# Kernel optimization log

Measured on AMD Instinct MI355X. Metric: run time of the kernel, lower is better.

The kernel has to match this reference:

```python
import jax, jax.numpy as jnp
import numpy as np

N, T, F_IN = 20000, 8, 64
FILTERS, HEADS = 32, 4
E = 320000
LEAKY = 0.2  # PyG GATConv default negative_slope
HID = HEADS * FILTERS  # 128


def setup_inputs() -> dict:
    key = jax.random.key(0)
    ks = jax.random.split(key, 16)
    g = lambda k, shape, scale: jax.random.normal(k, shape, dtype=jnp.float32) * scale
    return {
        "x": g(ks[0], (N, T, F_IN), 1.0),
        "edge_index": jax.random.randint(ks[1], (2, E), 0, N, dtype=jnp.int32),
        # GATConv 1: lin weight, attention vectors (per head), bias
        "W1": g(ks[2], (HID, F_IN), (2.0 / F_IN) ** 0.5),
        "att_src1": g(ks[3], (HEADS, FILTERS), 0.1),
        "att_dst1": g(ks[4], (HEADS, FILTERS), 0.1),
        "b1": jnp.zeros((HID,), jnp.float32),
        # GATConv 2
        "W2": g(ks[5], (HID, HID), (2.0 / HID) ** 0.5),
        "att_src2": g(ks[6], (HEADS, FILTERS), 0.1),
        "att_dst2": g(ks[7], (HEADS, FILTERS), 0.1),
        "b2": jnp.zeros((HID,), jnp.float32),
        # MLP head
        "lw1": g(ks[8], (FILTERS, HID), (2.0 / HID) ** 0.5),
        "lb1": jnp.zeros((FILTERS,), jnp.float32),
        "lw2": g(ks[9], (1, FILTERS), (2.0 / FILTERS) ** 0.5),
        "lb2": jnp.zeros((1,), jnp.float32),
    }


def gat_layer(x, src, dst, W, a_src, a_dst, b):
    """PyG GATConv (concat=True, add_self_loops already applied to src/dst)."""
    h = (x @ W.T).reshape(N, HEADS, FILTERS)          # [N,H,F]
    es = (h * a_src).sum(-1)                          # [N,H] per-node src score
    ed = (h * a_dst).sum(-1)                          # [N,H] per-node dst score
    e = jax.nn.leaky_relu(es[src] + ed[dst], LEAKY)   # [E',H]
    # segment softmax over incoming edges per destination node
    m = jax.ops.segment_max(e, dst, num_segments=N)
    ex = jnp.exp(e - m[dst])
    denom = jax.ops.segment_sum(ex, dst, num_segments=N)
    alpha = ex / (denom[dst] + 1e-16)                 # [E',H]
    out = jax.ops.segment_sum(h[src] * alpha[:, :, None], dst, num_segments=N)
    return out.reshape(N, HID) + b


def reference(x, edge_index, W1, att_src1, att_dst1, b1,
              W2, att_src2, att_dst2, b2, lw1, lb1, lw2, lb2):
    # add self loops (PyG GATConv default add_self_loops=True)
    loop = jnp.arange(N, dtype=edge_index.dtype)
    src = jnp.concatenate([edge_index[0], loop])
    dst = jnp.concatenate([edge_index[1], loop])

    def step(_, x_t):
        h = jax.nn.elu(gat_layer(x_t, src, dst, W1, att_src1, att_dst1, b1))
        # dropout is identity in eval mode
        h = jax.nn.elu(gat_layer(h, src, dst, W2, att_src2, att_dst2, b2))
        h = jax.nn.relu(h @ lw1.T + lb1)
        y = h @ lw2.T + lb2                            # [N,1]
        return None, y

    _, ys = jax.lax.scan(step, None, jnp.transpose(x, (1, 0, 2)))  # scan over T
    return ys  # [T, N, 1] (stacked version of the original list of outputs)
```

## Files before the change

kernel.cpp:

```cpp
#include <hip/hip_runtime.h>

constexpr int cN     = 20000;
constexpr int cT     = 8;
constexpr int cFIN   = 64;
constexpr int cHEADS = 4;
constexpr int cF     = 32;
constexpr int cHID   = 128;
constexpr int cE     = 320000;
constexpr int cET    = cE + cN;
constexpr int cR     = cN * cT;
constexpr float cLEAKY = 0.2f;

typedef __attribute__((ext_vector_type(8))) short bf16x8;
typedef __attribute__((ext_vector_type(4))) float f32x4;

static __device__ __forceinline__ unsigned short f2bfu(float f) {
    unsigned int u;
    __builtin_memcpy(&u, &f, 4);
    u += 0x7FFFu + ((u >> 16) & 1u);
    return (unsigned short)(u >> 16);
}
static __device__ __forceinline__ void unpack2(unsigned int v, float& lo, float& hi) {
    unsigned int ul = v << 16, uh = v & 0xFFFF0000u;
    __builtin_memcpy(&lo, &ul, 4);
    __builtin_memcpy(&hi, &uh, 4);
}
static __device__ __forceinline__ unsigned int pack2(float lo, float hi) {
    unsigned int ul, uh;
    __builtin_memcpy(&ul, &lo, 4);
    __builtin_memcpy(&uh, &hi, 4);
    ul += 0x7FFFu + ((ul >> 16) & 1u);
    uh += 0x7FFFu + ((uh >> 16) & 1u);
    return (ul >> 16) | (uh & 0xFFFF0000u);
}

__global__ void cvt_w_kernel(const float* W1, const float* W2, const float* lw1,
                             unsigned short* W1b, unsigned short* W2b, unsigned short* lw1b) {
    int i = blockIdx.x * 256 + threadIdx.x;
    if (i < cHID * cFIN)                      W1b[i] = f2bfu(W1[i]);
    else if (i < cHID * cFIN + cHID * cHID)   W2b[i - cHID * cFIN] = f2bfu(W2[i - cHID * cFIN]);
    else if (i < cHID * cFIN + cHID * cHID + cF * cHID)
        lw1b[i - cHID * cFIN - cHID * cHID] = f2bfu(lw1[i - cHID * cFIN - cHID * cHID]);
}

__global__ void deg_init_kernel(int* deg) {
    int n = blockIdx.x * blockDim.x + threadIdx.x;
    if (n < cN) deg[n] = 1;
}
__global__ void deg_count_kernel(const int* ei, int* deg) {
    int e = blockIdx.x * blockDim.x + threadIdx.x;
    if (e < cE) atomicAdd(&deg[ei[cE + e]], 1);
}
__global__ void scan_kernel(const int* deg, int* offs, int* cur) {
    __shared__ int lds[256];
    const int CH = 80;
    int tid  = threadIdx.x;
    int base = tid * CH;
    int tot = 0;
    for (int j = 0; j < CH; j++) {
        int idx = base + j;
        if (idx < cN) tot += deg[idx];
    }
    lds[tid] = tot;
    __syncthreads();
    for (int off = 1; off < 256; off <<= 1) {
        int v = (tid >= off) ? lds[tid - off] : 0;
        __syncthreads();
        lds[tid] += v;
        __syncthreads();
    }
    int run = lds[tid] - tot;
    for (int j = 0; j < CH; j++) {
        int idx = base + j;
        if (idx < cN) { offs[idx] = run; cur[idx] = run; run += deg[idx]; }
    }
    if (tid == 255) offs[cN] = lds[255];
}
__global__ void scatter_kernel(const int* ei, int* cur, int* csr) {
    int e = blockIdx.x * blockDim.x + threadIdx.x;
    if (e >= cET) return;
    int s, d;
    if (e < cE) { s = ei[e]; d = ei[cE + e]; }
    else        { s = e - cE; d = s; }
    int pos = atomicAdd(&cur[d], 1);
    csr[pos] = s;
}

__global__ __launch_bounds__(256) void gemm1_fused_kernel(
        const float* __restrict__ x, const unsigned short* __restrict__ W,
        const float* __restrict__ a_src, const float* __restrict__ a_dst,
        unsigned short* __restrict__ hb, float* __restrict__ es, float* __restrict__ ed) {
    __shared__ float hl[64][132];
    int tid  = threadIdx.x;
    int wave = tid >> 6;
    int lane = tid & 63;
    int q    = lane >> 4;
    int mi   = lane & 15;
    int m0   = blockIdx.x * 64 + wave * 16;

    int rho = m0 + mi;
    int t = rho / cN;
    int n = rho - t * cN;
    const float* xr = x + (size_t)n * (cT * cFIN) + t * cFIN;

    bf16x8 afrag[2];
    #pragma unroll
    for (int s = 0; s < 2; s++) {
        float4 v0 = *(const float4*)(xr + s * 32 + q * 8);
        float4 v1 = *(const float4*)(xr + s * 32 + q * 8 + 4);
        bf16x8 f;
        f[0] = (short)f2bfu(v0.x); f[1] = (short)f2bfu(v0.y);
        f[2] = (short)f2bfu(v0.z); f[3] = (short)f2bfu(v0.w);
        f[4] = (short)f2bfu(v1.x); f[5] = (short)f2bfu(v1.y);
        f[6] = (short)f2bfu(v1.z); f[7] = (short)f2bfu(v1.w);
        afrag[s] = f;
    }

    f32x4 acc[8];
    #pragma unroll
    for (int ct = 0; ct < 8; ct++) acc[ct] = (f32x4){0.f, 0.f, 0.f, 0.f};
    #pragma unroll
    for (int ct = 0; ct < 8; ct++) {
        int c = ct * 16 + mi;
        #pragma unroll
        for (int s = 0; s < 2; s++) {
            bf16x8 bfrag = *(const bf16x8*)(W + (size_t)c * cFIN + s * 32 + q * 8);
            acc[ct] = __builtin_amdgcn_mfma_f32_16x16x32_bf16(afrag[s], bfrag, acc[ct], 0, 0, 0);
        }
    }

    #pragma unroll
    for (int ct = 0; ct < 8; ct++)
        #pragma unroll
        for (int r = 0; r < 4; r++)
            hl[wave * 16 + q * 4 + r][ct * 16 + mi] = acc[ct][r];
    __syncthreads();

    {
        int r2 = tid & 63;
        int hd = tid >> 6;
        int rg = blockIdx.x * 64 + r2;
        const float* hr = &hl[r2][hd * cF];
        const float* sa = a_src + hd * cF;
        const float* da = a_dst + hd * cF;
        float s1 = 0.f, s2 = 0.f;
        #pragma unroll 8
        for (int f = 0; f < cF; f++) {
            float hv = hr[f];
            s1 += hv * sa[f];
            s2 += hv * da[f];
        }
        es[rg * cHEADS + hd] = s1;
        ed[rg * cHEADS + hd] = s2;
    }

    size_t base = (size_t)blockIdx.x * 64 * cHID;
    #pragma unroll
    for (int it = 0; it < 8; it++) {
        int g   = tid + it * 256;
        int row = g >> 5;
        int c4  = (g & 31) * 4;
        float4 v = *(const float4*)&hl[row][c4];
        unsigned int p0 = pack2(v.x, v.y), p1 = pack2(v.z, v.w);
        *(uint2*)(hb + base + (size_t)row * cHID + c4) = make_uint2(p0, p1);
    }
}

__global__ __launch_bounds__(256) void gemm2_mfma_kernel(
        const unsigned short* __restrict__ A, const unsigned short* __restrict__ W,
        const float* __restrict__ a_src, const float* __restrict__ a_dst,
        unsigned short* __restrict__ hb, float* __restrict__ es, float* __restrict__ ed) {
    __shared__ float hl[64][132];
    int tid  = threadIdx.x;
    int wave = tid >> 6;
    int lane = tid & 63;
    int q    = lane >> 4;
    int mi   = lane & 15;
    int m0   = blockIdx.x * 64 + wave * 16;

    bf16x8 afrag[4];
    #pragma unroll
    for (int s = 0; s < 4; s++)
        afrag[s] = *(const bf16x8*)(A + (size_t)(m0 + mi) * cHID + s * 32 + q * 8);

    f32x4 acc[8];
    #pragma unroll
    for (int ct = 0; ct < 8; ct++) acc[ct] = (f32x4){0.f, 0.f, 0.f, 0.f};
    #pragma unroll
    for (int ct = 0; ct < 8; ct++) {
        int c = ct * 16 + mi;
        #pragma unroll
        for (int s = 0; s < 4; s++) {
            bf16x8 bfrag = *(const bf16x8*)(W + (size_t)c * cHID + s * 32 + q * 8);
            acc[ct] = __builtin_amdgcn_mfma_f32_16x16x32_bf16(afrag[s], bfrag, acc[ct], 0, 0, 0);
        }
    }

    #pragma unroll
    for (int ct = 0; ct < 8; ct++)
        #pragma unroll
        for (int r = 0; r < 4; r++)
            hl[wave * 16 + q * 4 + r][ct * 16 + mi] = acc[ct][r];
    __syncthreads();

    {
        int r2 = tid & 63;
        int hd = tid >> 6;
        int rg = blockIdx.x * 64 + r2;
        const float* hr = &hl[r2][hd * cF];
        const float* sa = a_src + hd * cF;
        const float* da = a_dst + hd * cF;
        float s1 = 0.f, s2 = 0.f;
        #pragma unroll 8
        for (int f = 0; f < cF; f++) {
            float hv = hr[f];
            s1 += hv * sa[f];
            s2 += hv * da[f];
        }
        es[rg * cHEADS + hd] = s1;
        ed[rg * cHEADS + hd] = s2;
    }

    size_t base = (size_t)blockIdx.x * 64 * cHID;
    #pragma unroll
    for (int it = 0; it < 8; it++) {
        int g   = tid + it * 256;
        int row = g >> 5;
        int c4  = (g & 31) * 4;
        float4 v = *(const float4*)&hl[row][c4];
        unsigned int p0 = pack2(v.x, v.y), p1 = pack2(v.z, v.w);
        *(uint2*)(hb + base + (size_t)row * cHID + c4) = make_uint2(p0, p1);
    }
}

__global__ __launch_bounds__(256) void agg_kernel(
        const unsigned short* __restrict__ hb, const float* __restrict__ es,
        const float* __restrict__ ed,
        const int* __restrict__ offs, const int* __restrict__ csr,
        const float* __restrict__ bias, unsigned short* __restrict__ outb) {
    int b    = blockIdx.x;
    int t    = b & 7;
    int g    = b >> 3;
    int lrow = threadIdx.x >> 4;
    int n    = g * 16 + lrow;
    int j    = threadIdx.x & 15;
    int head = j >> 2;
    int rho  = t * cN + n;
    int s0 = offs[n], s1 = offs[n + 1];
    float edn = ed[(size_t)rho * cHEADS + head];
    const char* hpc = (const char*)(hb + (size_t)t * cN * cHID);
    const char* epc = (const char*)(es + (size_t)t * cN * cHEADS);
    const char* cc  = (const char*)csr;
    unsigned jo = (unsigned)j * 16u;
    unsigned ho = (unsigned)head * 4u;

    float acc[8] = {};
    float den = 0.f;
    int i = s0;
    for (; i + 3 < s1; i += 4) {
        unsigned io = (unsigned)i * 4u;
        int sa = *(const int*)(cc + io);
        int sb = *(const int*)(cc + io + 4u);
        int sc = *(const int*)(cc + io + 8u);
        int sd = *(const int*)(cc + io + 12u);
        uint4 ra = *(const uint4*)(hpc + (((unsigned)sa) << 8) + jo);
        uint4 rb = *(const uint4*)(hpc + (((unsigned)sb) << 8) + jo);
        uint4 rc = *(const uint4*)(hpc + (((unsigned)sc) << 8) + jo);
        uint4 rd = *(const uint4*)(hpc + (((unsigned)sd) << 8) + jo);
        float ea = *(const float*)(epc + (((unsigned)sa) << 4) + ho) + edn;
        float eb = *(const float*)(epc + (((unsigned)sb) << 4) + ho) + edn;
        float ec = *(const float*)(epc + (((unsigned)sc) << 4) + ho) + edn;
        float ee = *(const float*)(epc + (((unsigned)sd) << 4) + ho) + edn;
        ea = (ea >= 0.f) ? ea : cLEAKY * ea;
        eb = (eb >= 0.f) ? eb : cLEAKY * eb;
        ec = (ec >= 0.f) ? ec : cLEAKY * ec;
        ee = (ee >= 0.f) ? ee : cLEAKY * ee;
        float wa = __expf(ea), wb = __expf(eb), wc = __expf(ec), wd = __expf(ee);
        den += wa; den += wb; den += wc; den += wd;
        float lo, hi;
        unpack2(ra.x, lo, hi); acc[0] += wa * lo; acc[1] += wa * hi;
        unpack2(ra.y, lo, hi); acc[2] += wa * lo; acc[3] += wa * hi;
        unpack2(ra.z, lo, hi); acc[4] += wa * lo; acc[5] += wa * hi;
        unpack2(ra.w, lo, hi); acc[6] += wa * lo; acc[7] += wa * hi;
        unpack2(rb.x, lo, hi); acc[0] += wb * lo; acc[1] += wb * hi;
        unpack2(rb.y, lo, hi); acc[2] += wb * lo; acc[3] += wb * hi;
        unpack2(rb.z, lo, hi); acc[4] += wb * lo; acc[5] += wb * hi;
        unpack2(rb.w, lo, hi); acc[6] += wb * lo; acc[7] += wb * hi;
        unpack2(rc.x, lo, hi); acc[0] += wc * lo; acc[1] += wc * hi;
        unpack2(rc.y, lo, hi); acc[2] += wc * lo; acc[3] += wc * hi;
        unpack2(rc.z, lo, hi); acc[4] += wc * lo; acc[5] += wc * hi;
        unpack2(rc.w, lo, hi); acc[6] += wc * lo; acc[7] += wc * hi;
        unpack2(rd.x, lo, hi); acc[0] += wd * lo; acc[1] += wd * hi;
        unpack2(rd.y, lo, hi); acc[2] += wd * lo; acc[3] += wd * hi;
        unpack2(rd.z, lo, hi); acc[4] += wd * lo; acc[5] += wd * hi;
        unpack2(rd.w, lo, hi); acc[6] += wd * lo; acc[7] += wd * hi;
    }
    for (; i < s1; i++) {
        int sa = *(const int*)(cc + (unsigned)i * 4u);
        uint4 ra = *(const uint4*)(hpc + (((unsigned)sa) << 8) + jo);
        float ea = *(const float*)(epc + (((unsigned)sa) << 4) + ho) + edn;
        ea = (ea >= 0.f) ? ea : cLEAKY * ea;
        float wa = __expf(ea);
        den += wa;
        float lo, hi;
        unpack2(ra.x, lo, hi); acc[0] += wa * lo; acc[1] += wa * hi;
        unpack2(ra.y, lo, hi); acc[2] += wa * lo; acc[3] += wa * hi;
        unpack2(ra.z, lo, hi); acc[4] += wa * lo; acc[5] += wa * hi;
        unpack2(ra.w, lo, hi); acc[6] += wa * lo; acc[7] += wa * hi;
    }
    float inv = 1.f / (den + 1e-16f);
    float4 b0 = *(const float4*)(bias + 8 * j);
    float4 b1 = *(const float4*)(bias + 8 * j + 4);
    float r0 = acc[0] * inv + b0.x; r0 = (r0 > 0.f) ? r0 : expm1f(r0);
    float r1 = acc[1] * inv + b0.y; r1 = (r1 > 0.f) ? r1 : expm1f(r1);
    float r2 = acc[2] * inv + b0.z; r2 = (r2 > 0.f) ? r2 : expm1f(r2);
    float r3 = acc[3] * inv + b0.w; r3 = (r3 > 0.f) ? r3 : expm1f(r3);
    float r4 = acc[4] * inv + b1.x; r4 = (r4 > 0.f) ? r4 : expm1f(r4);
    float r5 = acc[5] * inv + b1.y; r5 = (r5 > 0.f) ? r5 : expm1f(r5);
    float r6 = acc[6] * inv + b1.z; r6 = (r6 > 0.f) ? r6 : expm1f(r6);
    float r7 = acc[7] * inv + b1.w; r7 = (r7 > 0.f) ? r7 : expm1f(r7);
    uint4 o;
    o.x = pack2(r0, r1); o.y = pack2(r2, r3); o.z = pack2(r4, r5); o.w = pack2(r6, r7);
    *(uint4*)(outb + (size_t)rho * cHID + 8 * j) = o;
}

__global__ __launch_bounds__(256) void TemporalGAT_20005957665499_kernel(
        const unsigned short* __restrict__ X, const unsigned short* __restrict__ lw1b,
        const float* __restrict__ lb1, const float* __restrict__ lw2,
        const float* __restrict__ lb2, float* __restrict__ out) {
    int tid  = threadIdx.x;
    int wave = tid >> 6;
    int lane = tid & 63;
    int q    = lane >> 4;
    int mi   = lane & 15;
    int m0   = blockIdx.x * 64 + wave * 16;

    bf16x8 afrag[4];
    #pragma unroll
    for (int s = 0; s < 4; s++)
        afrag[s] = *(const bf16x8*)(X + (size_t)(m0 + mi) * cHID + s * 32 + q * 8);

    f32x4 acc[2];
    acc[0] = (f32x4){0.f, 0.f, 0.f, 0.f};
    acc[1] = (f32x4){0.f, 0.f, 0.f, 0.f};
    #pragma unroll
    for (int ct = 0; ct < 2; ct++) {
        int c = ct * 16 + mi;
        #pragma unroll
        for (int s = 0; s < 4; s++) {
            bf16x8 bfrag = *(const bf16x8*)(lw1b + (size_t)c * cHID + s * 32 + q * 8);
            acc[ct] = __builtin_amdgcn_mfma_f32_16x16x32_bf16(afrag[s], bfrag, acc[ct], 0, 0, 0);
        }
    }

    float lb1a = lb1[mi], lb1b_ = lb1[16 + mi];
    float lw2a = lw2[mi], lw2b_ = lw2[16 + mi];
    float l2 = lb2[0];
    #pragma unroll
    for (int r = 0; r < 4; r++) {
        float va = acc[0][r] + lb1a; va = fmaxf(va, 0.f);
        float vb = acc[1][r] + lb1b_; vb = fmaxf(vb, 0.f);
        float v = va * lw2a + vb * lw2b_;
        v += __shfl_xor(v, 1);
        v += __shfl_xor(v, 2);
        v += __shfl_xor(v, 4);
        v += __shfl_xor(v, 8);
        if (mi == 0) out[m0 + q * 4 + r] = v + l2;
    }
}

extern "C" void kernel_launch(void* const* d_in, const int* in_sizes, int n_in,
                              void* d_out, int out_size, void* d_ws, size_t ws_size,
                              hipStream_t stream) {
    const float* x   = (const float*)d_in[0];
    const int*   ei  = (const int*)d_in[1];
    const float* W1  = (const float*)d_in[2];
    const float* as1 = (const float*)d_in[3];
    const float* ad1 = (const float*)d_in[4];
    const float* b1  = (const float*)d_in[5];
    const float* W2  = (const float*)d_in[6];
    const float* as2 = (const float*)d_in[7];
    const float* ad2 = (const float*)d_in[8];
    const float* b2  = (const float*)d_in[9];
    const float* lw1 = (const float*)d_in[10];
    const float* lb1 = (const float*)d_in[11];
    const float* lw2 = (const float*)d_in[12];
    const float* lb2 = (const float*)d_in[13];
    float* out = (float*)d_out;
    (void)in_sizes; (void)n_in; (void)out_size; (void)ws_size;

    char* ws = (char*)d_ws;
    size_t o = 0;
    auto carveN = [&](size_t bytes) { void* p = ws + o; o += (bytes + 255) & ~(size_t)255; return p; };
    unsigned short* hb   = (unsigned short*)carveN((size_t)cR * cHID * 2);
    unsigned short* xb2  = (unsigned short*)carveN((size_t)cR * cHID * 2);
    unsigned short* xb3  = (unsigned short*)carveN((size_t)cR * cHID * 2);
    unsigned short* W1b  = (unsigned short*)carveN((size_t)cHID * cFIN * 2);
    unsigned short* W2b  = (unsigned short*)carveN((size_t)cHID * cHID * 2);
    unsigned short* lw1b = (unsigned short*)carveN((size_t)cF * cHID * 2);
    float* es_buf  = (float*)carveN((size_t)cR * cHEADS * 4);
    float* ed_buf  = (float*)carveN((size_t)cR * cHEADS * 4);
    int*   deg     = (int*)carveN((size_t)cN * 4);
    int*   offs    = (int*)carveN((size_t)(cN + 1) * 4);
    int*   cursor  = (int*)carveN((size_t)cN * 4);
    int*   csr     = (int*)carveN((size_t)cET * 4);

    cvt_w_kernel<<<(cHID * cFIN + cHID * cHID + cF * cHID + 255) / 256, 256, 0, stream>>>(
        W1, W2, lw1, W1b, W2b, lw1b);

    deg_init_kernel<<<(cN + 255) / 256, 256, 0, stream>>>(deg);
    deg_count_kernel<<<(cE + 255) / 256, 256, 0, stream>>>(ei, deg);
    scan_kernel<<<1, 256, 0, stream>>>(deg, offs, cursor);
    scatter_kernel<<<(cET + 255) / 256, 256, 0, stream>>>(ei, cursor, csr);

    gemm1_fused_kernel<<<cR / 64, 256, 0, stream>>>(x, W1b, as1, ad1, hb, es_buf, ed_buf);
    agg_kernel<<<(cN / 16) * cT, 256, 0, stream>>>(hb, es_buf, ed_buf, offs, csr, b1, xb2);
    gemm2_mfma_kernel<<<cR / 64, 256, 0, stream>>>(xb2, W2b, as2, ad2, hb, es_buf, ed_buf);
    agg_kernel<<<(cN / 16) * cT, 256, 0, stream>>>(hb, es_buf, ed_buf, offs, csr, b2, xb3);
    TemporalGAT_20005957665499_kernel<<<cR / 64, 256, 0, stream>>>(xb3, lw1b, lb1, lw2, lb2, out);
}
```

Before: 415.6 us.

## Fuse GAT aggregation with following GEMM and MLP head, use exp2 scaling

Fuses each attention-aggregation pass with the next dense step: the layer-1 aggregation now feeds the layer-2 GEMM and score computation through a swizzled LDS tile, and the layer-2 aggregation feeds the MLP head directly. This removes two intermediate bf16 activation round trips through global memory and two kernel launches. Attention scores are pre-scaled by log2(e) so the inner loop uses the hardware exp2 instead of __expf. The degree scan is also staged through LDS, which costs about 80KB of shared memory in a single-block kernel. The fused kernels do small 16-row MFMA tiles per block, and the head kernel leaves three of four waves idle during its GEMM.

```diff
diff --git a/kernel.cpp b/kernel.cpp
--- a/kernel.cpp
+++ b/kernel.cpp
@@ -10,6 +10,7 @@
 constexpr int cET    = cE + cN;
 constexpr int cR     = cN * cT;
 constexpr float cLEAKY = 0.2f;
+constexpr float cL2E = 1.44269504088896340736f;
 
 typedef __attribute__((ext_vector_type(8))) short bf16x8;
 typedef __attribute__((ext_vector_type(4))) float f32x4;
@@ -52,15 +53,20 @@
     if (e < cE) atomicAdd(&deg[ei[cE + e]], 1);
 }
 __global__ void scan_kernel(const int* deg, int* offs, int* cur) {
+    __shared__ int sdeg[79 * 256];
     __shared__ int lds[256];
-    const int CH = 80;
-    int tid  = threadIdx.x;
+    int tid = threadIdx.x;
+    #pragma unroll 4
+    for (int k = 0; k < 79; k++) {
+        int idx = k * 256 + tid;
+        sdeg[idx] = (idx < cN) ? deg[idx] : 0;
+    }
+    __syncthreads();
+    const int CH = 79;
     int base = tid * CH;
     int tot = 0;
-    for (int j = 0; j < CH; j++) {
-        int idx = base + j;
-        if (idx < cN) tot += deg[idx];
-    }
+    #pragma unroll 8
+    for (int j = 0; j < CH; j++) tot += sdeg[base + j];
     lds[tid] = tot;
     __syncthreads();
     for (int off = 1; off < 256; off <<= 1) {
@@ -72,7 +78,7 @@
     int run = lds[tid] - tot;
     for (int j = 0; j < CH; j++) {
         int idx = base + j;
-        if (idx < cN) { offs[idx] = run; cur[idx] = run; run += deg[idx]; }
+        if (idx < cN) { offs[idx] = run; cur[idx] = run; run += sdeg[idx]; }
     }
     if (tid == 255) offs[cN] = lds[255];
 }
@@ -150,8 +156,8 @@
             s1 += hv * sa[f];
             s2 += hv * da[f];
         }
-        es[rg * cHEADS + hd] = s1;
-        ed[rg * cHEADS + hd] = s2;
+        es[rg * cHEADS + hd] = s1 * cL2E;
+        ed[rg * cHEADS + hd] = s2 * cL2E;
     }
 
     size_t base = (size_t)blockIdx.x * 64 * cHID;
@@ -166,84 +172,11 @@
     }
 }
 
-__global__ __launch_bounds__(256) void gemm2_mfma_kernel(
-        const unsigned short* __restrict__ A, const unsigned short* __restrict__ W,
-        const float* __restrict__ a_src, const float* __restrict__ a_dst,
-        unsigned short* __restrict__ hb, float* __restrict__ es, float* __restrict__ ed) {
-    __shared__ float hl[64][132];
-    int tid  = threadIdx.x;
-    int wave = tid >> 6;
-    int lane = tid & 63;
-    int q    = lane >> 4;
-    int mi   = lane & 15;
-    int m0   = blockIdx.x * 64 + wave * 16;
-
-    bf16x8 afrag[4];
-    #pragma unroll
-    for (int s = 0; s < 4; s++)
-        afrag[s] = *(const bf16x8*)(A + (size_t)(m0 + mi) * cHID + s * 32 + q * 8);
-
-    f32x4 acc[8];
-    #pragma unroll
-    for (int ct = 0; ct < 8; ct++) acc[ct] = (f32x4){0.f, 0.f, 0.f, 0.f};
-    #pragma unroll
-    for (int ct = 0; ct < 8; ct++) {
-        int c = ct * 16 + mi;
-        #pragma unroll
-        for (int s = 0; s < 4; s++) {
-            bf16x8 bfrag = *(const bf16x8*)(W + (size_t)c * cHID + s * 32 + q * 8);
-            acc[ct] = __builtin_amdgcn_mfma_f32_16x16x32_bf16(afrag[s], bfrag, acc[ct], 0, 0, 0);
-        }
-    }
-
-    #pragma unroll
-    for (int ct = 0; ct < 8; ct++)
-        #pragma unroll
-        for (int r = 0; r < 4; r++)
-            hl[wave * 16 + q * 4 + r][ct * 16 + mi] = acc[ct][r];
-    __syncthreads();
-
-    {
-        int r2 = tid & 63;
-        int hd = tid >> 6;
-        int rg = blockIdx.x * 64 + r2;
-        const float* hr = &hl[r2][hd * cF];
-        const float* sa = a_src + hd * cF;
-        const float* da = a_dst + hd * cF;
-        float s1 = 0.f, s2 = 0.f;
-        #pragma unroll 8
-        for (int f = 0; f < cF; f++) {
-            float hv = hr[f];
-            s1 += hv * sa[f];
-            s2 += hv * da[f];
-        }
-        es[rg * cHEADS + hd] = s1;
-        ed[rg * cHEADS + hd] = s2;
-    }
-
-    size_t base = (size_t)blockIdx.x * 64 * cHID;
-    #pragma unroll
-    for (int it = 0; it < 8; it++) {
-        int g   = tid + it * 256;
-        int row = g >> 5;
-        int c4  = (g & 31) * 4;
-        float4 v = *(const float4*)&hl[row][c4];
-        unsigned int p0 = pack2(v.x, v.y), p1 = pack2(v.z, v.w);
-        *(uint2*)(hb + base + (size_t)row * cHID + c4) = make_uint2(p0, p1);
-    }
-}
-
-__global__ __launch_bounds__(256) void agg_kernel(
+static __device__ __forceinline__ void agg_core(
         const unsigned short* __restrict__ hb, const float* __restrict__ es,
-        const float* __restrict__ ed,
-        const int* __restrict__ offs, const int* __restrict__ csr,
-        const float* __restrict__ bias, unsigned short* __restrict__ outb) {
-    int b    = blockIdx.x;
-    int t    = b & 7;
-    int g    = b >> 3;
-    int lrow = threadIdx.x >> 4;
-    int n    = g * 16 + lrow;
-    int j    = threadIdx.x & 15;
+        const float* __restrict__ ed, const int* __restrict__ offs,
+        const int* __restrict__ csr, const float* __restrict__ bias,
+        int t, int n, int j, float* r) {
     int head = j >> 2;
     int rho  = t * cN + n;
     int s0 = offs[n], s1 = offs[n + 1];
@@ -275,7 +208,8 @@
         eb = (eb >= 0.f) ? eb : cLEAKY * eb;
         ec = (ec >= 0.f) ? ec : cLEAKY * ec;
         ee = (ee >= 0.f) ? ee : cLEAKY * ee;
-        float wa = __expf(ea), wb = __expf(eb), wc = __expf(ec), wd = __expf(ee);
+        float wa = __builtin_amdgcn_exp2f(ea), wb = __builtin_amdgcn_exp2f(eb);
+        float wc = __builtin_amdgcn_exp2f(ec), wd = __builtin_amdgcn_exp2f(ee);
         den += wa; den += wb; den += wc; den += wd;
         float lo, hi;
         unpack2(ra.x, lo, hi); acc[0] += wa * lo; acc[1] += wa * hi;
@@ -300,7 +234,7 @@
         uint4 ra = *(const uint4*)(hpc + (((unsigned)sa) << 8) + jo);
         float ea = *(const float*)(epc + (((unsigned)sa) << 4) + ho) + edn;
         ea = (ea >= 0.f) ? ea : cLEAKY * ea;
-        float wa = __expf(ea);
+        float wa = __builtin_amdgcn_exp2f(ea);
         den += wa;
         float lo, hi;
         unpack2(ra.x, lo, hi); acc[0] += wa * lo; acc[1] += wa * hi;
@@ -310,62 +244,167 @@
     }
     float inv = 1.f / (den + 1e-16f);
     float4 b0 = *(const float4*)(bias + 8 * j);
-    float4 b1 = *(const float4*)(bias + 8 * j + 4);
-    float r0 = acc[0] * inv + b0.x; r0 = (r0 > 0.f) ? r0 : expm1f(r0);
-    float r1 = acc[1] * inv + b0.y; r1 = (r1 > 0.f) ? r1 : expm1f(r1);
-    float r2 = acc[2] * inv + b0.z; r2 = (r2 > 0.f) ? r2 : expm1f(r2);
-    float r3 = acc[3] * inv + b0.w; r3 = (r3 > 0.f) ? r3 : expm1f(r3);
-    float r4 = acc[4] * inv + b1.x; r4 = (r4 > 0.f) ? r4 : expm1f(r4);
-    float r5 = acc[5] * inv + b1.y; r5 = (r5 > 0.f) ? r5 : expm1f(r5);
-    float r6 = acc[6] * inv + b1.z; r6 = (r6 > 0.f) ? r6 : expm1f(r6);
-    float r7 = acc[7] * inv + b1.w; r7 = (r7 > 0.f) ? r7 : expm1f(r7);
-    uint4 o;
-    o.x = pack2(r0, r1); o.y = pack2(r2, r3); o.z = pack2(r4, r5); o.w = pack2(r6, r7);
-    *(uint4*)(outb + (size_t)rho * cHID + 8 * j) = o;
-}
-
-__global__ __launch_bounds__(256) void TemporalGAT_20005957665499_kernel(
-        const unsigned short* __restrict__ X, const unsigned short* __restrict__ lw1b,
-        const float* __restrict__ lb1, const float* __restrict__ lw2,
-        const float* __restrict__ lb2, float* __restrict__ out) {
+    float4 b1v = *(const float4*)(bias + 8 * j + 4);
+    float v0 = acc[0] * inv + b0.x;  r[0] = (v0 > 0.f) ? v0 : expm1f(v0);
+    float v1 = acc[1] * inv + b0.y;  r[1] = (v1 > 0.f) ? v1 : expm1f(v1);
+    float v2 = acc[2] * inv + b0.z;  r[2] = (v2 > 0.f) ? v2 : expm1f(v2);
+    float v3 = acc[3] * inv + b0.w;  r[3] = (v3 > 0.f) ? v3 : expm1f(v3);
+    float v4 = acc[4] * inv + b1v.x; r[4] = (v4 > 0.f) ? v4 : expm1f(v4);
+    float v5 = acc[5] * inv + b1v.y; r[5] = (v5 > 0.f) ? v5 : expm1f(v5);
+    float v6 = acc[6] * inv + b1v.z; r[6] = (v6 > 0.f) ? v6 : expm1f(v6);
+    float v7 = acc[7] * inv + b1v.w; r[7] = (v7 > 0.f) ? v7 : expm1f(v7);
+}
+
+__global__ __launch_bounds__(256) void agg_gemm_kernel(
+        const unsigned short* __restrict__ hb, const float* __restrict__ es,
+        const float* __restrict__ ed, const int* __restrict__ offs,
+        const int* __restrict__ csr, const float* __restrict__ bias,
+        const unsigned short* __restrict__ W2, const float* __restrict__ a_src,
+        const float* __restrict__ a_dst, unsigned short* __restrict__ hb2,
+        float* __restrict__ es2, float* __restrict__ ed2) {
+    __shared__ unsigned short tile[16 * 128];
+    __shared__ float hl[16][132];
+    int b    = blockIdx.x;
+    int t    = b & 7;
+    int g    = b >> 3;
     int tid  = threadIdx.x;
+    int lrow = tid >> 4;
+    int j    = tid & 15;
+    int n0   = g * 16;
+
+    float r[8];
+    agg_core(hb, es, ed, offs, csr, bias, t, n0 + lrow, j, r);
+    {
+        uint4 o;
+        o.x = pack2(r[0], r[1]); o.y = pack2(r[2], r[3]);
+        o.z = pack2(r[4], r[5]); o.w = pack2(r[6], r[7]);
+        unsigned tb = (unsigned)lrow * 256u + (((unsigned)j * 16u) ^ (((unsigned)(lrow & 7)) << 4));
+        *(uint4*)((char*)tile + tb) = o;
+    }
+    __syncthreads();
+
     int wave = tid >> 6;
     int lane = tid & 63;
     int q    = lane >> 4;
     int mi   = lane & 15;
-    int m0   = blockIdx.x * 64 + wave * 16;
-
     bf16x8 afrag[4];
     #pragma unroll
-    for (int s = 0; s < 4; s++)
-        afrag[s] = *(const bf16x8*)(X + (size_t)(m0 + mi) * cHID + s * 32 + q * 8);
-
-    f32x4 acc[2];
-    acc[0] = (f32x4){0.f, 0.f, 0.f, 0.f};
-    acc[1] = (f32x4){0.f, 0.f, 0.f, 0.f};
+    for (int s = 0; s < 4; s++) {
+        unsigned addr = (unsigned)mi * 256u +
+                        (((unsigned)(s * 64 + q * 16)) ^ (((unsigned)(mi & 7)) << 4));
+        afrag[s] = *(const bf16x8*)((const char*)tile + addr);
+    }
+    f32x4 acc2[2];
+    acc2[0] = (f32x4){0.f, 0.f, 0.f, 0.f};
+    acc2[1] = (f32x4){0.f, 0.f, 0.f, 0.f};
     #pragma unroll
     for (int ct = 0; ct < 2; ct++) {
-        int c = ct * 16 + mi;
+        int c = (wave * 2 + ct) * 16 + mi;
         #pragma unroll
         for (int s = 0; s < 4; s++) {
-            bf16x8 bfrag = *(const bf16x8*)(lw1b + (size_t)c * cHID + s * 32 + q * 8);
-            acc[ct] = __builtin_amdgcn_mfma_f32_16x16x32_bf16(afrag[s], bfrag, acc[ct], 0, 0, 0);
-        }
-    }
-
-    float lb1a = lb1[mi], lb1b_ = lb1[16 + mi];
-    float lw2a = lw2[mi], lw2b_ = lw2[16 + mi];
-    float l2 = lb2[0];
-    #pragma unroll
-    for (int r = 0; r < 4; r++) {
-        float va = acc[0][r] + lb1a; va = fmaxf(va, 0.f);
-        float vb = acc[1][r] + lb1b_; vb = fmaxf(vb, 0.f);
-        float v = va * lw2a + vb * lw2b_;
-        v += __shfl_xor(v, 1);
-        v += __shfl_xor(v, 2);
-        v += __shfl_xor(v, 4);
-        v += __shfl_xor(v, 8);
-        if (mi == 0) out[m0 + q * 4 + r] = v + l2;
+            bf16x8 bfrag = *(const bf16x8*)(W2 + (size_t)c * cHID + s * 32 + q * 8);
+            acc2[ct] = __builtin_amdgcn_mfma_f32_16x16x32_bf16(afrag[s], bfrag, acc2[ct], 0, 0, 0);
+        }
+    }
+    #pragma unroll
+    for (int ct = 0; ct < 2; ct++)
+        #pragma unroll
+        for (int rr = 0; rr < 4; rr++)
+            hl[q * 4 + rr][(wave * 2 + ct) * 16 + mi] = acc2[ct][rr];
+    __syncthreads();
+
+    if (tid < 64) {
+        int r2 = tid & 15;
+        int hd = tid >> 4;
+        int rg = t * cN + n0 + r2;
+        const float* hr = &hl[r2][hd * cF];
+        const float* sa = a_src + hd * cF;
+        const float* da = a_dst + hd * cF;
+        float s1 = 0.f, s2 = 0.f;
+        #pragma unroll 8
+        for (int f = 0; f < cF; f++) {
+            float hv = hr[f];
+            s1 += hv * sa[f];
+            s2 += hv * da[f];
+        }
+        es2[(size_t)rg * cHEADS + hd] = s1 * cL2E;
+        ed2[(size_t)rg * cHEADS + hd] = s2 * cL2E;
+    }
+    {
+        int row = tid >> 4;
+        int c8  = (tid & 15) * 8;
+        float4 v0 = *(const float4*)&hl[row][c8];
+        float4 v1 = *(const float4*)&hl[row][c8 + 4];
+        uint4 o;
+        o.x = pack2(v0.x, v0.y); o.y = pack2(v0.z, v0.w);
+        o.z = pack2(v1.x, v1.y); o.w = pack2(v1.z, v1.w);
+        *(uint4*)(hb2 + (size_t)(t * cN + n0 + row) * cHID + c8) = o;
+    }
+}
+
+__global__ __launch_bounds__(256) void TemporalGAT_20005957665499_kernel(
+        const unsigned short* __restrict__ hb2, const float* __restrict__ es,
+        const float* __restrict__ ed, const int* __restrict__ offs,
+        const int* __restrict__ csr, const float* __restrict__ bias,
+        const unsigned short* __restrict__ lw1b, const float* __restrict__ lb1,
+        const float* __restrict__ lw2, const float* __restrict__ lb2,
+        float* __restrict__ out) {
+    __shared__ unsigned short tile[16 * 128];
+    int b    = blockIdx.x;
+    int t    = b & 7;
+    int g    = b >> 3;
+    int tid  = threadIdx.x;
+    int lrow = tid >> 4;
+    int j    = tid & 15;
+    int n0   = g * 16;
+
+    float r[8];
+    agg_core(hb2, es, ed, offs, csr, bias, t, n0 + lrow, j, r);
+    {
+        uint4 o;
+        o.x = pack2(r[0], r[1]); o.y = pack2(r[2], r[3]);
+        o.z = pack2(r[4], r[5]); o.w = pack2(r[6], r[7]);
+        unsigned tb = (unsigned)lrow * 256u + (((unsigned)j * 16u) ^ (((unsigned)(lrow & 7)) << 4));
+        *(uint4*)((char*)tile + tb) = o;
+    }
+    __syncthreads();
+
+    if (tid < 64) {
+        int q  = tid >> 4;
+        int mi = tid & 15;
+        bf16x8 afrag[4];
+        #pragma unroll
+        for (int s = 0; s < 4; s++) {
+            unsigned addr = (unsigned)mi * 256u +
+                            (((unsigned)(s * 64 + q * 16)) ^ (((unsigned)(mi & 7)) << 4));
+            afrag[s] = *(const bf16x8*)((const char*)tile + addr);
+        }
+        f32x4 acc2[2];
+        acc2[0] = (f32x4){0.f, 0.f, 0.f, 0.f};
+        acc2[1] = (f32x4){0.f, 0.f, 0.f, 0.f};
+        #pragma unroll
+        for (int ct = 0; ct < 2; ct++) {
+            int c = ct * 16 + mi;
+            #pragma unroll
+            for (int s = 0; s < 4; s++) {
+                bf16x8 bfrag = *(const bf16x8*)(lw1b + (size_t)c * cHID + s * 32 + q * 8);
+                acc2[ct] = __builtin_amdgcn_mfma_f32_16x16x32_bf16(afrag[s], bfrag, acc2[ct], 0, 0, 0);
+            }
+        }
+        float lb1a = lb1[mi], lb1b_ = lb1[16 + mi];
+        float lw2a = lw2[mi], lw2b_ = lw2[16 + mi];
+        float l2 = lb2[0];
+        #pragma unroll
+        for (int rr = 0; rr < 4; rr++) {
+            float va = fmaxf(acc2[0][rr] + lb1a, 0.f);
+            float vb = fmaxf(acc2[1][rr] + lb1b_, 0.f);
+            float v = va * lw2a + vb * lw2b_;
+            v += __shfl_xor(v, 1);
+            v += __shfl_xor(v, 2);
+            v += __shfl_xor(v, 4);
+            v += __shfl_xor(v, 8);
+            if (mi == 0) out[t * cN + n0 + q * 4 + rr] = v + l2;
+        }
     }
 }
 
@@ -393,13 +432,14 @@
     size_t o = 0;
     auto carveN = [&](size_t bytes) { void* p = ws + o; o += (bytes + 255) & ~(size_t)255; return p; };
     unsigned short* hb   = (unsigned short*)carveN((size_t)cR * cHID * 2);
-    unsigned short* xb2  = (unsigned short*)carveN((size_t)cR * cHID * 2);
-    unsigned short* xb3  = (unsigned short*)carveN((size_t)cR * cHID * 2);
+    unsigned short* hb2  = (unsigned short*)carveN((size_t)cR * cHID * 2);
     unsigned short* W1b  = (unsigned short*)carveN((size_t)cHID * cFIN * 2);
     unsigned short* W2b  = (unsigned short*)carveN((size_t)cHID * cHID * 2);
     unsigned short* lw1b = (unsigned short*)carveN((size_t)cF * cHID * 2);
-    float* es_buf  = (float*)carveN((size_t)cR * cHEADS * 4);
-    float* ed_buf  = (float*)carveN((size_t)cR * cHEADS * 4);
+    float* es1_buf = (float*)carveN((size_t)cR * cHEADS * 4);
+    float* ed1_buf = (float*)carveN((size_t)cR * cHEADS * 4);
+    float* es2_buf = (float*)carveN((size_t)cR * cHEADS * 4);
+    float* ed2_buf = (float*)carveN((size_t)cR * cHEADS * 4);
     int*   deg     = (int*)carveN((size_t)cN * 4);
     int*   offs    = (int*)carveN((size_t)(cN + 1) * 4);
     int*   cursor  = (int*)carveN((size_t)cN * 4);
@@ -413,9 +453,9 @@
     scan_kernel<<<1, 256, 0, stream>>>(deg, offs, cursor);
     scatter_kernel<<<(cET + 255) / 256, 256, 0, stream>>>(ei, cursor, csr);
 
-    gemm1_fused_kernel<<<cR / 64, 256, 0, stream>>>(x, W1b, as1, ad1, hb, es_buf, ed_buf);
-    agg_kernel<<<(cN / 16) * cT, 256, 0, stream>>>(hb, es_buf, ed_buf, offs, csr, b1, xb2);
-    gemm2_mfma_kernel<<<cR / 64, 256, 0, stream>>>(xb2, W2b, as2, ad2, hb, es_buf, ed_buf);
-    agg_kernel<<<(cN / 16) * cT, 256, 0, stream>>>(hb, es_buf, ed_buf, offs, csr, b2, xb3);
-    TemporalGAT_20005957665499_kernel<<<cR / 64, 256, 0, stream>>>(xb3, lw1b, lb1, lw2, lb2, out);
-}
+    gemm1_fused_kernel<<<cR / 64, 256, 0, stream>>>(x, W1b, as1, ad1, hb, es1_buf, ed1_buf);
+    agg_gemm_kernel<<<(cN / 16) * cT, 256, 0, stream>>>(
+        hb, es1_buf, ed1_buf, offs, csr, b1, W2b, as2, ad2, hb2, es2_buf, ed2_buf);
+    TemporalGAT_20005957665499_kernel<<<(cN / 16) * cT, 256, 0, stream>>>(
+        hb2, es2_buf, ed2_buf, offs, csr, b2, lw1b, lb1, lw2, lb2, out);
+}
```

After: 382.8 us. 7.9% less time.
